# Optimization experiments

Hardware: AMD Instinct MI355X
Metric: run time of the kernel (lower is better)

Reference implementation:

```python
import jax, jax.numpy as jnp
import numpy as np

N, E, IN, HID, OUT = 100000, 1600000, 128, 128, 64


def _gcn(x, w, b, src, dst, norm, n):
    # PyG GCNConv: linear transform, then normalized scatter-add aggregation
    h = x @ w                                  # [N, F_out]
    msg = h[src] * norm[:, None]               # gather + scale, [E', F_out]
    agg = jax.ops.segment_sum(msg, dst, num_segments=n)
    return agg + b


def setup_inputs() -> dict:
    key = jax.random.key(0)
    ks = jax.random.split(key, 10)
    s = 0.05
    return {
        "X": jax.random.normal(ks[0], (N, IN), jnp.float32),
        "edge_index": jax.random.randint(ks[1], (2, E), 0, N, jnp.int64),
        "unused": 0,
        "gw1": jax.random.normal(ks[2], (IN, HID), jnp.float32) * s,
        "gb1": jnp.zeros((HID,), jnp.float32),
        "lw1": jax.random.normal(ks[3], (IN, HID), jnp.float32) * s,
        "lb1": jnp.zeros((HID,), jnp.float32),
        "gw2": jax.random.normal(ks[4], (HID, HID), jnp.float32) * s,
        "gb2": jnp.zeros((HID,), jnp.float32),
        "lw2": jax.random.normal(ks[5], (HID, HID), jnp.float32) * s,
        "lb2": jnp.zeros((HID,), jnp.float32),
        "gw3": jax.random.normal(ks[6], (HID, HID), jnp.float32) * s,
        "gb3": jnp.zeros((HID,), jnp.float32),
        "lw3": jax.random.normal(ks[7], (HID, HID), jnp.float32) * s,
        "lb3": jnp.zeros((HID,), jnp.float32),
        "fcw": jax.random.normal(ks[8], (HID, OUT), jnp.float32) * s,
        "fcb": jnp.zeros((OUT,), jnp.float32),
    }


def reference(X, edge_index, unused, gw1, gb1, lw1, lb1, gw2, gb2, lw2, lb2,
              gw3, gb3, lw3, lb3, fcw, fcb):
    n = X.shape[0]
    loop = jnp.arange(n)
    src = jnp.concatenate([edge_index[0], loop])   # self-loops appended
    dst = jnp.concatenate([edge_index[1], loop])
    deg = jax.ops.segment_sum(jnp.ones_like(dst, dtype=X.dtype), dst, num_segments=n)
    dis = jnp.where(deg > 0, jax.lax.rsqrt(jnp.maximum(deg, 1e-12)), 0.0)
    norm = dis[src] * dis[dst]                     # D^-1/2 (A+I) D^-1/2 weights

    lrelu = lambda v: jax.nn.leaky_relu(v, negative_slope=0.01)
    h = lrelu(_gcn(X, gw1, gb1, src, dst, norm, n) + X @ lw1 + lb1)
    h = lrelu(_gcn(h, gw2, gb2, src, dst, norm, n) + h @ lw2 + lb2)
    h = lrelu(_gcn(h, gw3, gb3, src, dst, norm, n) + h @ lw3 + lb3)
    y = h @ fcw + fcb
    return (h, y)
```

## Files before the change

### kernel.cpp

```cpp
#include <hip/hip_runtime.h>
#include <cstdint>
#include <cstddef>


typedef __attribute__((ext_vector_type(4))) float f32x4;
typedef __attribute__((ext_vector_type(8))) short bf16x8;
typedef unsigned short u16;

#define G_CHUNKS 256

__device__ __forceinline__ float bf2f(unsigned int u) {
  union { unsigned int i; float f; } v;
  v.i = u << 16;
  return v.f;
}
__device__ __forceinline__ u16 f2bf(float f) {
  union { float f; unsigned int i; } v;
  v.f = f;
  unsigned int i = v.i;
  return (u16)((i + 0x7FFFu + ((i >> 16) & 1u)) >> 16);
}


__global__ __launch_bounds__(256) void k_hist(const int* __restrict__ ei,
                                              int* __restrict__ ghist,
                                              int E, int B, int chunk) {
  __shared__ int h[512];
  for (int t = threadIdx.x; t < B; t += 256) h[t] = 0;
  __syncthreads();
  const int g = blockIdx.x;
  const int beg = g * chunk;
  const int end = min(beg + chunk, E);
  for (int e = beg + threadIdx.x; e < end; e += 256)
    atomicAdd(&h[ei[E + e] >> 8], 1);
  __syncthreads();
  for (int t = threadIdx.x; t < B; t += 256) ghist[(size_t)t * G_CHUNKS + g] = h[t];
}

__global__ __launch_bounds__(256) void k_hscan(int* __restrict__ ghist,
                                               int* __restrict__ btot) {
  __shared__ int sm[256];
  int* p = ghist + (size_t)blockIdx.x * G_CHUNKS;
  const int t = threadIdx.x;
  int v = p[t];
  sm[t] = v;
  __syncthreads();
  for (int off = 1; off < 256; off <<= 1) {
    int u = (t >= off) ? sm[t - off] : 0;
    __syncthreads();
    sm[t] += u;
    __syncthreads();
  }
  p[t] = sm[t] - v;
  if (t == 255) btot[blockIdx.x] = sm[255];
}

__global__ __launch_bounds__(512) void k_bscan(const int* __restrict__ btot,
                                               int* __restrict__ boff, int B,
                                               int* __restrict__ rowptr, int n,
                                               int E, int tot) {
  __shared__ int sm[512];
  const int t = threadIdx.x;
  int v = (t < B) ? btot[t] : 0;
  sm[t] = v;
  __syncthreads();
  for (int off = 1; off < 512; off <<= 1) {
    int u = (t >= off) ? sm[t - off] : 0;
    __syncthreads();
    sm[t] += u;
    __syncthreads();
  }
  if (t < B) boff[t] = sm[t] - v;
  if (t == 0) {
    boff[B] = E;
    rowptr[n] = tot;
  }
}

__global__ __launch_bounds__(256) void k_scatter(const int* __restrict__ ei,
                                                 const int* __restrict__ ghist,
                                                 const int* __restrict__ boff,
                                                 unsigned int* __restrict__ ebuf,
                                                 int E, int B, int chunk) {
  __shared__ int off[512];
  const int g = blockIdx.x;
  for (int t = threadIdx.x; t < B; t += 256)
    off[t] = boff[t] + ghist[(size_t)t * G_CHUNKS + g];
  __syncthreads();
  const int beg = g * chunk;
  const int end = min(beg + chunk, E);
  for (int e = beg + threadIdx.x; e < end; e += 256) {
    int s = ei[e];
    int d = ei[E + e];
    int pos = atomicAdd(&off[d >> 8], 1);
    ebuf[pos] = ((unsigned int)s << 8) | (unsigned int)(d & 255);
  }
}

__global__ __launch_bounds__(256) void k_cfill(const unsigned int* __restrict__ ebuf,
                                               const int* __restrict__ boff,
                                               int* __restrict__ rowptr,
                                               int* __restrict__ col,
                                               float* __restrict__ dis, int n) {
  __shared__ int cnt[256];
  __shared__ int fl[256];
  const int b = blockIdx.x;
  const int t = threadIdx.x;
  const int beg = boff[b];
  const int end = boff[b + 1];
  const int node0 = b << 8;
  const int nn = min(256, n - node0);
  cnt[t] = 0;
  __syncthreads();
  for (int e = beg + t; e < end; e += 256)
    atomicAdd(&cnt[ebuf[e] & 255u], 1);
  __syncthreads();
  int v = cnt[t];
  __shared__ int sm[256];
  sm[t] = v;
  __syncthreads();
  for (int off = 1; off < 256; off <<= 1) {
    int u = (t >= off) ? sm[t - off] : 0;
    __syncthreads();
    sm[t] += u;
    __syncthreads();
  }
  if (t < nn) {
    int excl = sm[t] - v;
    int rbase = beg + node0 + t + excl;
    int i = node0 + t;
    rowptr[i] = rbase;
    col[rbase] = i;
    fl[t] = rbase + 1;
    dis[i] = rsqrtf((float)(v + 1));
  }
  __syncthreads();
  for (int e = beg + t; e < end; e += 256) {
    unsigned int pk = ebuf[e];
    int pos = atomicAdd(&fl[pk & 255u], 1);
    col[pos] = (int)(pk >> 8);
  }
}


__global__ __launch_bounds__(256) void k_cvt(const float* __restrict__ src,
                                             const float* __restrict__ dis,
                                             u16* __restrict__ dstb,
                                             u16* __restrict__ dsts, int total8) {
  int i = blockIdx.x * 256 + threadIdx.x;
  if (i >= total8) return;
  size_t b = (size_t)i * 8;
  float ds = dis[i >> 4];
  float4 a0 = *(const float4*)(src + b);
  float4 a1 = *(const float4*)(src + b + 4);
  u16 ob[8] = {f2bf(a0.x), f2bf(a0.y), f2bf(a0.z), f2bf(a0.w),
               f2bf(a1.x), f2bf(a1.y), f2bf(a1.z), f2bf(a1.w)};
  u16 os[8] = {f2bf(a0.x * ds), f2bf(a0.y * ds), f2bf(a0.z * ds), f2bf(a0.w * ds),
               f2bf(a1.x * ds), f2bf(a1.y * ds), f2bf(a1.z * ds), f2bf(a1.w * ds)};
  *(ulonglong2*)(dstb + b) = *(ulonglong2*)ob;
  *(ulonglong2*)(dsts + b) = *(ulonglong2*)os;
}

__global__ __launch_bounds__(128) void k_prep(const float* __restrict__ w0,
                                              const float* __restrict__ w1,
                                              const float* __restrict__ w2,
                                              const float* __restrict__ w3,
                                              const float* __restrict__ w4,
                                              const float* __restrict__ w5,
                                              const float* __restrict__ g1,
                                              const float* __restrict__ l1,
                                              const float* __restrict__ g2,
                                              const float* __restrict__ l2,
                                              const float* __restrict__ g3,
                                              const float* __restrict__ l3,
                                              const float* __restrict__ fcw,
                                              u16* __restrict__ wt,
                                              float* __restrict__ bias,
                                              u16* __restrict__ fcT) {
  int bx = blockIdx.x;
  if (bx < 768) {
    int z = bx >> 7, nr = bx & 127, k = threadIdx.x;
    const float* Ws[6] = {w0, w1, w2, w3, w4, w5};
    wt[(size_t)z * 16384 + nr * 128 + k] = f2bf(Ws[z][k * 128 + nr]);
  } else if (bx < 771) {
    int t = (bx - 768) * 128 + threadIdx.x;
    if (t < 384) {
      const float* gs[3] = {g1, g2, g3};
      const float* ls[3] = {l1, l2, l3};
      bias[t] = gs[t >> 7][t & 127] + ls[t >> 7][t & 127];
    }
  } else {
    int nr = bx - 771;
    int k = threadIdx.x;
    fcT[nr * 128 + k] = f2bf(fcw[k * 64 + nr]);
  }
}

__global__ __launch_bounds__(256, 8) void k_spmv_bf(const int* __restrict__ rowptr,
                                                    const int* __restrict__ col,
                                                    const float* __restrict__ dis,
                                                    const u16* __restrict__ Xs,
                                                    u16* __restrict__ SXb, int n) {
  const int tid = threadIdx.x;
  const int half = (tid >> 5) & 1;
  const int sub = tid & 31;
  const int i = blockIdx.x * 8 + (tid >> 6) * 2 + half;
  if (i >= n) return;
  int j = rowptr[i];
  const int end = rowptr[i + 1];
  float a0 = 0.f, a1 = 0.f, a2 = 0.f, a3 = 0.f;

#define ROWQ(c) (*(const uint2*)(Xs + (size_t)(c) * 128 + sub * 4))
#define ACC(q)  do { uint2 _q = (q); \
                     a0 += bf2f(_q.x & 0xffffu); a1 += bf2f(_q.x >> 16); \
                     a2 += bf2f(_q.y & 0xffffu); a3 += bf2f(_q.y >> 16); } while (0)

  for (; (j & 3) && j < end; ++j) ACC(ROWQ(col[j]));
  for (; j + 7 < end; j += 8) {
    int4 c0 = *(const int4*)(col + j);
    int4 c1 = *(const int4*)(col + j + 4);
    uint2 q0 = ROWQ(c0.x), q1 = ROWQ(c0.y), q2 = ROWQ(c0.z), q3 = ROWQ(c0.w);
    uint2 q4 = ROWQ(c1.x), q5 = ROWQ(c1.y), q6 = ROWQ(c1.z), q7 = ROWQ(c1.w);
    ACC(q0); ACC(q1); ACC(q2); ACC(q3);
    ACC(q4); ACC(q5); ACC(q6); ACC(q7);
  }
  if (j + 3 < end) {
    int4 c0 = *(const int4*)(col + j);
    uint2 q0 = ROWQ(c0.x), q1 = ROWQ(c0.y), q2 = ROWQ(c0.z), q3 = ROWQ(c0.w);
    ACC(q0); ACC(q1); ACC(q2); ACC(q3);
    j += 4;
  }
  for (; j < end; ++j) ACC(ROWQ(col[j]));
#undef ROWQ
#undef ACC

  const float di = dis[i];
  uint2 o;
  o.x = (unsigned int)f2bf(a0 * di) | ((unsigned int)f2bf(a1 * di) << 16);
  o.y = (unsigned int)f2bf(a2 * di) | ((unsigned int)f2bf(a3 * di) << 16);
  *(uint2*)(SXb + (size_t)i * 128 + sub * 4) = o;
}

__global__ __launch_bounds__(256, 8) void k_mfma(const u16* __restrict__ A0,
                                                 const u16* __restrict__ A1,
                                                 const u16* __restrict__ W0T,
                                                 const u16* __restrict__ W1T,
                                                 const float* __restrict__ bias,
                                                 const float* __restrict__ dis,
                                                 u16* __restrict__ outb,
                                                 u16* __restrict__ outs,
                                                 float* __restrict__ outf, int M) {
  const int lane = threadIdx.x & 63;
  const int wv = threadIdx.x >> 6;
  const int row0 = blockIdx.x * 128 + wv * 32;
  const int c0off = blockIdx.y * 32;
  const int r = lane & 15;
  const int kg = lane >> 4;

  f32x4 acc[2][2];
#pragma unroll
  for (int a = 0; a < 2; ++a)
#pragma unroll
    for (int j = 0; j < 2; ++j) acc[a][j] = (f32x4){0.f, 0.f, 0.f, 0.f};

  const int ra0 = min(row0 + r, M - 1);
  const int ra1 = min(row0 + 16 + r, M - 1);

#pragma unroll
  for (int p = 0; p < 2; ++p) {
    const u16* A = p ? A1 : A0;
    const u16* WT = p ? W1T : W0T;
#pragma unroll
    for (int kk = 0; kk < 4; ++kk) {
      const int k0 = kk * 32 + kg * 8;
      bf16x8 a0 = *(const bf16x8*)(A + (size_t)ra0 * 128 + k0);
      bf16x8 a1 = *(const bf16x8*)(A + (size_t)ra1 * 128 + k0);
#pragma unroll
      for (int j = 0; j < 2; ++j) {
        bf16x8 b = *(const bf16x8*)(WT + (size_t)(c0off + j * 16 + r) * 128 + k0);
        acc[0][j] = __builtin_amdgcn_mfma_f32_16x16x32_bf16(a0, b, acc[0][j], 0, 0, 0);
        acc[1][j] = __builtin_amdgcn_mfma_f32_16x16x32_bf16(a1, b, acc[1][j], 0, 0, 0);
      }
    }
  }

#pragma unroll
  for (int rf = 0; rf < 2; ++rf)
#pragma unroll
    for (int e = 0; e < 4; ++e) {
      const int row = row0 + rf * 16 + kg * 4 + e;
      if (row >= M) continue;
      const float ds = outs ? dis[row] : 0.f;
#pragma unroll
      for (int j = 0; j < 2; ++j) {
        const int c = c0off + j * 16 + r;
        float v = acc[rf][j][e] + bias[c];
        v = (v > 0.f) ? v : 0.01f * v;
        if (outf) outf[(size_t)row * 128 + c] = v;
        if (outb) outb[(size_t)row * 128 + c] = f2bf(v);
        if (outs) outs[(size_t)row * 128 + c] = f2bf(v * ds);
      }
    }
}

__global__ __launch_bounds__(256) void k_fc_mfma(const u16* __restrict__ hb3,
                                                 const u16* __restrict__ fcT,
                                                 const float* __restrict__ fcb,
                                                 float* __restrict__ y, int M) {
  const int lane = threadIdx.x & 63;
  const int wv = threadIdx.x >> 6;
  const int row0 = blockIdx.x * 128 + wv * 32;
  const int r = lane & 15;
  const int kg = lane >> 4;

  f32x4 acc[2][4];
#pragma unroll
  for (int a = 0; a < 2; ++a)
#pragma unroll
    for (int j = 0; j < 4; ++j) acc[a][j] = (f32x4){0.f, 0.f, 0.f, 0.f};

  const int ra0 = min(row0 + r, M - 1);
  const int ra1 = min(row0 + 16 + r, M - 1);

#pragma unroll
  for (int kk = 0; kk < 4; ++kk) {
    const int k0 = kk * 32 + kg * 8;
    bf16x8 a0 = *(const bf16x8*)(hb3 + (size_t)ra0 * 128 + k0);
    bf16x8 a1 = *(const bf16x8*)(hb3 + (size_t)ra1 * 128 + k0);
#pragma unroll
    for (int j = 0; j < 4; ++j) {
      bf16x8 b = *(const bf16x8*)(fcT + (size_t)(j * 16 + r) * 128 + k0);
      acc[0][j] = __builtin_amdgcn_mfma_f32_16x16x32_bf16(a0, b, acc[0][j], 0, 0, 0);
      acc[1][j] = __builtin_amdgcn_mfma_f32_16x16x32_bf16(a1, b, acc[1][j], 0, 0, 0);
    }
  }

#pragma unroll
  for (int rf = 0; rf < 2; ++rf)
#pragma unroll
    for (int e = 0; e < 4; ++e) {
      const int row = row0 + rf * 16 + kg * 4 + e;
      if (row >= M) continue;
#pragma unroll
      for (int j = 0; j < 4; ++j) {
        const int c = j * 16 + r;
        y[(size_t)row * 64 + c] = acc[rf][j][e] + fcb[c];
      }
    }
}


extern "C" void kernel_launch(void* const* d_in, const int* in_sizes, int n_in,
                              void* d_out, int out_size, void* d_ws, size_t ws_size,
                              hipStream_t stream) {
  const float* X  = (const float*)d_in[0];
  const int* ei   = (const int*)d_in[1];
  const float* gw1 = (const float*)d_in[3];
  const float* gb1 = (const float*)d_in[4];
  const float* lw1 = (const float*)d_in[5];
  const float* lb1 = (const float*)d_in[6];
  const float* gw2 = (const float*)d_in[7];
  const float* gb2 = (const float*)d_in[8];
  const float* lw2 = (const float*)d_in[9];
  const float* lb2 = (const float*)d_in[10];
  const float* gw3 = (const float*)d_in[11];
  const float* gb3 = (const float*)d_in[12];
  const float* lw3 = (const float*)d_in[13];
  const float* lb3 = (const float*)d_in[14];
  const float* fcw = (const float*)d_in[15];
  const float* fcb = (const float*)d_in[16];

  const int n = in_sizes[0] / 128;
  const int E = in_sizes[1] / 2;
  const int tot = E + n;
  const int B = (n + 255) >> 8;
  const int chunk = (E + G_CHUNKS - 1) / G_CHUNKS;

  char* ws = (char*)d_ws;
  size_t off = 0;
  auto alloc = [&](size_t bytes) -> void* {
    void* p = ws + off;
    off = (off + bytes + 255) & ~(size_t)255;
    return p;
  };
  int* ghist   = (int*)alloc((size_t)B * G_CHUNKS * 4);
  int* btot    = (int*)alloc(512 * 4);
  int* boff    = (int*)alloc((size_t)(B + 1) * 4);
  int* rowptr  = (int*)alloc((size_t)(n + 1) * 4);
  float* dis   = (float*)alloc((size_t)n * 4);
  int* col     = (int*)alloc((size_t)tot * 4);
  unsigned int* ebuf = (unsigned int*)alloc((size_t)E * 4);
  u16* Xb      = (u16*)alloc((size_t)n * 128 * 2);
  u16* Xs      = (u16*)alloc((size_t)n * 128 * 2);
  u16* SXb     = (u16*)alloc((size_t)n * 128 * 2);
  u16* WT      = (u16*)alloc((size_t)6 * 16384 * 2);
  u16* fcT     = (u16*)alloc((size_t)64 * 128 * 2);
  float* bias  = (float*)alloc(384 * 4);

  float* outh = (float*)d_out;
  float* outy = outh + (size_t)n * 128;
  u16* hb = (u16*)outy;

  const int gM = (n + 127) / 128;
  const int gW = (n + 7) / 8;
  const int g8 = (n * 128 / 8 + 255) / 256;

  k_hist<<<G_CHUNKS, 256, 0, stream>>>(ei, ghist, E, B, chunk);
  k_hscan<<<B, 256, 0, stream>>>(ghist, btot);
  k_bscan<<<1, 512, 0, stream>>>(btot, boff, B, rowptr, n, E, tot);
  k_scatter<<<G_CHUNKS, 256, 0, stream>>>(ei, ghist, boff, ebuf, E, B, chunk);
  k_cfill<<<B, 256, 0, stream>>>(ebuf, boff, rowptr, col, dis, n);

  k_cvt<<<g8, 256, 0, stream>>>(X, dis, Xb, Xs, n * 128 / 8);
  k_prep<<<835, 128, 0, stream>>>(gw1, lw1, gw2, lw2, gw3, lw3,
                                  gb1, lb1, gb2, lb2, gb3, lb3, fcw,
                                  WT, bias, fcT);

  k_spmv_bf<<<gW, 256, 0, stream>>>(rowptr, col, dis, Xs, SXb, n);
  k_mfma<<<dim3(gM, 4), 256, 0, stream>>>(SXb, Xb, WT, WT + 16384, bias, dis,
                                          hb, Xs, nullptr, n);
  k_spmv_bf<<<gW, 256, 0, stream>>>(rowptr, col, dis, Xs, SXb, n);
  k_mfma<<<dim3(gM, 4), 256, 0, stream>>>(SXb, hb, WT + 2 * 16384, WT + 3 * 16384,
                                          bias + 128, dis, Xb, Xs, nullptr, n);
  k_spmv_bf<<<gW, 256, 0, stream>>>(rowptr, col, dis, Xs, SXb, n);
  k_mfma<<<dim3(gM, 4), 256, 0, stream>>>(SXb, Xb, WT + 4 * 16384, WT + 5 * 16384,
                                          bias + 256, dis, hb, nullptr, outh, n);
  k_fc_mfma<<<gM, 256, 0, stream>>>(hb, fcT, fcb, outy, n);
}
```

Before: 443.0 us.

## Store only degree-scaled bf16 activations and recover unscaled values via sqrt(deg)

Drops the separate unscaled bf16 activation copy. Each layer now writes only the dis-scaled bf16 tensor. The self-linear term is computed from the scaled tensor and multiplied by sqrt(deg) in the epilogue, with separate accumulators, and the final fc applies the same rescale. The SpMV is also changed to 16 lanes per row with 16-byte gathers instead of 32 lanes with 8-byte gathers. This cuts a full bf16 write per layer and the extra conversion output, at the cost of extra rounding error from scaling before bf16 quantisation.

After: 602.7 us. 36.0% more time.

```diff
diff --git a/kernel.cpp b/kernel.cpp
--- a/kernel.cpp
+++ b/kernel.cpp
@@ -101,7 +101,8 @@
                                                const int* __restrict__ boff,
                                                int* __restrict__ rowptr,
                                                int* __restrict__ col,
-                                               float* __restrict__ dis, int n) {
+                                               float* __restrict__ dis,
+                                               float* __restrict__ idis, int n) {
   __shared__ int cnt[256];
   __shared__ int fl[256];
   const int b = blockIdx.x;
@@ -132,7 +133,9 @@
     rowptr[i] = rbase;
     col[rbase] = i;
     fl[t] = rbase + 1;
-    dis[i] = rsqrtf((float)(v + 1));
+    float dv = (float)(v + 1);
+    dis[i] = rsqrtf(dv);
+    idis[i] = sqrtf(dv);
   }
   __syncthreads();
   for (int e = beg + t; e < end; e += 256) {
@@ -145,7 +148,6 @@
 
 __global__ __launch_bounds__(256) void k_cvt(const float* __restrict__ src,
                                              const float* __restrict__ dis,
-                                             u16* __restrict__ dstb,
                                              u16* __restrict__ dsts, int total8) {
   int i = blockIdx.x * 256 + threadIdx.x;
   if (i >= total8) return;
@@ -153,11 +155,8 @@
   float ds = dis[i >> 4];
   float4 a0 = *(const float4*)(src + b);
   float4 a1 = *(const float4*)(src + b + 4);
-  u16 ob[8] = {f2bf(a0.x), f2bf(a0.y), f2bf(a0.z), f2bf(a0.w),
-               f2bf(a1.x), f2bf(a1.y), f2bf(a1.z), f2bf(a1.w)};
   u16 os[8] = {f2bf(a0.x * ds), f2bf(a0.y * ds), f2bf(a0.z * ds), f2bf(a0.w * ds),
                f2bf(a1.x * ds), f2bf(a1.y * ds), f2bf(a1.z * ds), f2bf(a1.w * ds)};
-  *(ulonglong2*)(dstb + b) = *(ulonglong2*)ob;
   *(ulonglong2*)(dsts + b) = *(ulonglong2*)os;
 }
 
@@ -202,31 +201,33 @@
                                                     const u16* __restrict__ Xs,
                                                     u16* __restrict__ SXb, int n) {
   const int tid = threadIdx.x;
-  const int half = (tid >> 5) & 1;
-  const int sub = tid & 31;
-  const int i = blockIdx.x * 8 + (tid >> 6) * 2 + half;
+  const int sub = tid & 15;
+  const int i = blockIdx.x * 16 + (tid >> 4);
   if (i >= n) return;
   int j = rowptr[i];
   const int end = rowptr[i + 1];
   float a0 = 0.f, a1 = 0.f, a2 = 0.f, a3 = 0.f;
-
-#define ROWQ(c) (*(const uint2*)(Xs + (size_t)(c) * 128 + sub * 4))
-#define ACC(q)  do { uint2 _q = (q); \
+  float a4 = 0.f, a5 = 0.f, a6 = 0.f, a7 = 0.f;
+
+#define ROWQ(c) (*(const uint4*)(Xs + (size_t)(c) * 128 + sub * 8))
+#define ACC(q)  do { uint4 _q = (q); \
                      a0 += bf2f(_q.x & 0xffffu); a1 += bf2f(_q.x >> 16); \
-                     a2 += bf2f(_q.y & 0xffffu); a3 += bf2f(_q.y >> 16); } while (0)
+                     a2 += bf2f(_q.y & 0xffffu); a3 += bf2f(_q.y >> 16); \
+                     a4 += bf2f(_q.z & 0xffffu); a5 += bf2f(_q.z >> 16); \
+                     a6 += bf2f(_q.w & 0xffffu); a7 += bf2f(_q.w >> 16); } while (0)
 
   for (; (j & 3) && j < end; ++j) ACC(ROWQ(col[j]));
   for (; j + 7 < end; j += 8) {
     int4 c0 = *(const int4*)(col + j);
     int4 c1 = *(const int4*)(col + j + 4);
-    uint2 q0 = ROWQ(c0.x), q1 = ROWQ(c0.y), q2 = ROWQ(c0.z), q3 = ROWQ(c0.w);
-    uint2 q4 = ROWQ(c1.x), q5 = ROWQ(c1.y), q6 = ROWQ(c1.z), q7 = ROWQ(c1.w);
+    uint4 q0 = ROWQ(c0.x), q1 = ROWQ(c0.y), q2 = ROWQ(c0.z), q3 = ROWQ(c0.w);
+    uint4 q4 = ROWQ(c1.x), q5 = ROWQ(c1.y), q6 = ROWQ(c1.z), q7 = ROWQ(c1.w);
     ACC(q0); ACC(q1); ACC(q2); ACC(q3);
     ACC(q4); ACC(q5); ACC(q6); ACC(q7);
   }
   if (j + 3 < end) {
     int4 c0 = *(const int4*)(col + j);
-    uint2 q0 = ROWQ(c0.x), q1 = ROWQ(c0.y), q2 = ROWQ(c0.z), q3 = ROWQ(c0.w);
+    uint4 q0 = ROWQ(c0.x), q1 = ROWQ(c0.y), q2 = ROWQ(c0.z), q3 = ROWQ(c0.w);
     ACC(q0); ACC(q1); ACC(q2); ACC(q3);
     j += 4;
   }
@@ -235,19 +236,21 @@
 #undef ACC
 
   const float di = dis[i];
-  uint2 o;
+  uint4 o;
   o.x = (unsigned int)f2bf(a0 * di) | ((unsigned int)f2bf(a1 * di) << 16);
   o.y = (unsigned int)f2bf(a2 * di) | ((unsigned int)f2bf(a3 * di) << 16);
-  *(uint2*)(SXb + (size_t)i * 128 + sub * 4) = o;
+  o.z = (unsigned int)f2bf(a4 * di) | ((unsigned int)f2bf(a5 * di) << 16);
+  o.w = (unsigned int)f2bf(a6 * di) | ((unsigned int)f2bf(a7 * di) << 16);
+  *(uint4*)(SXb + (size_t)i * 128 + sub * 8) = o;
 }
 
 __global__ __launch_bounds__(256, 8) void k_mfma(const u16* __restrict__ A0,
-                                                 const u16* __restrict__ A1,
+                                                 const u16* __restrict__ A1s,
                                                  const u16* __restrict__ W0T,
                                                  const u16* __restrict__ W1T,
                                                  const float* __restrict__ bias,
                                                  const float* __restrict__ dis,
-                                                 u16* __restrict__ outb,
+                                                 const float* __restrict__ idis,
                                                  u16* __restrict__ outs,
                                                  float* __restrict__ outf, int M) {
   const int lane = threadIdx.x & 63;
@@ -257,30 +260,40 @@
   const int r = lane & 15;
   const int kg = lane >> 4;
 
-  f32x4 acc[2][2];
+  f32x4 accA[2][2], accB[2][2];
 #pragma unroll
   for (int a = 0; a < 2; ++a)
 #pragma unroll
-    for (int j = 0; j < 2; ++j) acc[a][j] = (f32x4){0.f, 0.f, 0.f, 0.f};
+    for (int j = 0; j < 2; ++j) {
+      accA[a][j] = (f32x4){0.f, 0.f, 0.f, 0.f};
+      accB[a][j] = (f32x4){0.f, 0.f, 0.f, 0.f};
+    }
 
   const int ra0 = min(row0 + r, M - 1);
   const int ra1 = min(row0 + 16 + r, M - 1);
 
 #pragma unroll
-  for (int p = 0; p < 2; ++p) {
-    const u16* A = p ? A1 : A0;
-    const u16* WT = p ? W1T : W0T;
-#pragma unroll
-    for (int kk = 0; kk < 4; ++kk) {
-      const int k0 = kk * 32 + kg * 8;
-      bf16x8 a0 = *(const bf16x8*)(A + (size_t)ra0 * 128 + k0);
-      bf16x8 a1 = *(const bf16x8*)(A + (size_t)ra1 * 128 + k0);
-#pragma unroll
-      for (int j = 0; j < 2; ++j) {
-        bf16x8 b = *(const bf16x8*)(WT + (size_t)(c0off + j * 16 + r) * 128 + k0);
-        acc[0][j] = __builtin_amdgcn_mfma_f32_16x16x32_bf16(a0, b, acc[0][j], 0, 0, 0);
-        acc[1][j] = __builtin_amdgcn_mfma_f32_16x16x32_bf16(a1, b, acc[1][j], 0, 0, 0);
-      }
+  for (int kk = 0; kk < 4; ++kk) {
+    const int k0 = kk * 32 + kg * 8;
+    bf16x8 a0 = *(const bf16x8*)(A0 + (size_t)ra0 * 128 + k0);
+    bf16x8 a1 = *(const bf16x8*)(A0 + (size_t)ra1 * 128 + k0);
+#pragma unroll
+    for (int j = 0; j < 2; ++j) {
+      bf16x8 b = *(const bf16x8*)(W0T + (size_t)(c0off + j * 16 + r) * 128 + k0);
+      accA[0][j] = __builtin_amdgcn_mfma_f32_16x16x32_bf16(a0, b, accA[0][j], 0, 0, 0);
+      accA[1][j] = __builtin_amdgcn_mfma_f32_16x16x32_bf16(a1, b, accA[1][j], 0, 0, 0);
+    }
+  }
+#pragma unroll
+  for (int kk = 0; kk < 4; ++kk) {
+    const int k0 = kk * 32 + kg * 8;
+    bf16x8 a0 = *(const bf16x8*)(A1s + (size_t)ra0 * 128 + k0);
+    bf16x8 a1 = *(const bf16x8*)(A1s + (size_t)ra1 * 128 + k0);
+#pragma unroll
+    for (int j = 0; j < 2; ++j) {
+      bf16x8 b = *(const bf16x8*)(W1T + (size_t)(c0off + j * 16 + r) * 128 + k0);
+      accB[0][j] = __builtin_amdgcn_mfma_f32_16x16x32_bf16(a0, b, accB[0][j], 0, 0, 0);
+      accB[1][j] = __builtin_amdgcn_mfma_f32_16x16x32_bf16(a1, b, accB[1][j], 0, 0, 0);
     }
   }
 
@@ -290,22 +303,23 @@
     for (int e = 0; e < 4; ++e) {
       const int row = row0 + rf * 16 + kg * 4 + e;
       if (row >= M) continue;
-      const float ds = outs ? dis[row] : 0.f;
+      const float ids = idis[row];
+      const float ds = dis[row];
 #pragma unroll
       for (int j = 0; j < 2; ++j) {
         const int c = c0off + j * 16 + r;
-        float v = acc[rf][j][e] + bias[c];
+        float v = accA[rf][j][e] + ids * accB[rf][j][e] + bias[c];
         v = (v > 0.f) ? v : 0.01f * v;
         if (outf) outf[(size_t)row * 128 + c] = v;
-        if (outb) outb[(size_t)row * 128 + c] = f2bf(v);
         if (outs) outs[(size_t)row * 128 + c] = f2bf(v * ds);
       }
     }
 }
 
-__global__ __launch_bounds__(256) void k_fc_mfma(const u16* __restrict__ hb3,
+__global__ __launch_bounds__(256) void k_fc_mfma(const u16* __restrict__ hs3,
                                                  const u16* __restrict__ fcT,
                                                  const float* __restrict__ fcb,
+                                                 const float* __restrict__ idis,
                                                  float* __restrict__ y, int M) {
   const int lane = threadIdx.x & 63;
   const int wv = threadIdx.x >> 6;
@@ -325,8 +339,8 @@
 #pragma unroll
   for (int kk = 0; kk < 4; ++kk) {
     const int k0 = kk * 32 + kg * 8;
-    bf16x8 a0 = *(const bf16x8*)(hb3 + (size_t)ra0 * 128 + k0);
-    bf16x8 a1 = *(const bf16x8*)(hb3 + (size_t)ra1 * 128 + k0);
+    bf16x8 a0 = *(const bf16x8*)(hs3 + (size_t)ra0 * 128 + k0);
+    bf16x8 a1 = *(const bf16x8*)(hs3 + (size_t)ra1 * 128 + k0);
 #pragma unroll
     for (int j = 0; j < 4; ++j) {
       bf16x8 b = *(const bf16x8*)(fcT + (size_t)(j * 16 + r) * 128 + k0);
@@ -341,10 +355,11 @@
     for (int e = 0; e < 4; ++e) {
       const int row = row0 + rf * 16 + kg * 4 + e;
       if (row >= M) continue;
+      const float ids = idis[row];
 #pragma unroll
       for (int j = 0; j < 4; ++j) {
         const int c = j * 16 + r;
-        y[(size_t)row * 64 + c] = acc[rf][j][e] + fcb[c];
+        y[(size_t)row * 64 + c] = ids * acc[rf][j][e] + fcb[c];
       }
     }
 }
@@ -388,9 +403,9 @@
   int* boff    = (int*)alloc((size_t)(B + 1) * 4);
   int* rowptr  = (int*)alloc((size_t)(n + 1) * 4);
   float* dis   = (float*)alloc((size_t)n * 4);
+  float* idis  = (float*)alloc((size_t)n * 4);
   int* col     = (int*)alloc((size_t)tot * 4);
   unsigned int* ebuf = (unsigned int*)alloc((size_t)E * 4);
-  u16* Xb      = (u16*)alloc((size_t)n * 128 * 2);
   u16* Xs      = (u16*)alloc((size_t)n * 128 * 2);
   u16* SXb     = (u16*)alloc((size_t)n * 128 * 2);
   u16* WT      = (u16*)alloc((size_t)6 * 16384 * 2);
@@ -402,28 +417,28 @@
   u16* hb = (u16*)outy;
 
   const int gM = (n + 127) / 128;
-  const int gW = (n + 7) / 8;
+  const int gW = (n + 15) / 16;
   const int g8 = (n * 128 / 8 + 255) / 256;
 
   k_hist<<<G_CHUNKS, 256, 0, stream>>>(ei, ghist, E, B, chunk);
   k_hscan<<<B, 256, 0, stream>>>(ghist, btot);
   k_bscan<<<1, 512, 0, stream>>>(btot, boff, B, rowptr, n, E, tot);
   k_scatter<<<G_CHUNKS, 256, 0, stream>>>(ei, ghist, boff, ebuf, E, B, chunk);
-  k_cfill<<<B, 256, 0, stream>>>(ebuf, boff, rowptr, col, dis, n);
-
-  k_cvt<<<g8, 256, 0, stream>>>(X, dis, Xb, Xs, n * 128 / 8);
+  k_cfill<<<B, 256, 0, stream>>>(ebuf, boff, rowptr, col, dis, idis, n);
+
+  k_cvt<<<g8, 256, 0, stream>>>(X, dis, Xs, n * 128 / 8);
   k_prep<<<835, 128, 0, stream>>>(gw1, lw1, gw2, lw2, gw3, lw3,
                                   gb1, lb1, gb2, lb2, gb3, lb3, fcw,
                                   WT, bias, fcT);
 
   k_spmv_bf<<<gW, 256, 0, stream>>>(rowptr, col, dis, Xs, SXb, n);
-  k_mfma<<<dim3(gM, 4), 256, 0, stream>>>(SXb, Xb, WT, WT + 16384, bias, dis,
-                                          hb, Xs, nullptr, n);
+  k_mfma<<<dim3(gM, 4), 256, 0, stream>>>(SXb, Xs, WT, WT + 16384, bias,
+                                          dis, idis, hb, nullptr, n);
+  k_spmv_bf<<<gW, 256, 0, stream>>>(rowptr, col, dis, hb, SXb, n);
+  k_mfma<<<dim3(gM, 4), 256, 0, stream>>>(SXb, hb, WT + 2 * 16384, WT + 3 * 16384,
+                                          bias + 128, dis, idis, Xs, nullptr, n);
   k_spmv_bf<<<gW, 256, 0, stream>>>(rowptr, col, dis, Xs, SXb, n);
-  k_mfma<<<dim3(gM, 4), 256, 0, stream>>>(SXb, hb, WT + 2 * 16384, WT + 3 * 16384,
-                                          bias + 128, dis, Xb, Xs, nullptr, n);
-  k_spmv_bf<<<gW, 256, 0, stream>>>(rowptr, col, dis, Xs, SXb, n);
-  k_mfma<<<dim3(gM, 4), 256, 0, stream>>>(SXb, Xb, WT + 4 * 16384, WT + 5 * 16384,
-                                          bias + 256, dis, hb, nullptr, outh, n);
-  k_fc_mfma<<<gM, 256, 0, stream>>>(hb, fcT, fcb, outy, n);
-}
+  k_mfma<<<dim3(gM, 4), 256, 0, stream>>>(SXb, Xs, WT + 4 * 16384, WT + 5 * 16384,
+                                          bias + 256, dis, idis, hb, outh, n);
+  k_fc_mfma<<<gM, 256, 0, stream>>>(hb, fcT, fcb, idis, outy, n);
+}
```
